# Optimization experiments

Hardware: AMD Instinct MI355X
Metric: run time of the kernel (lower is better)

The kernel has to match this reference:

```python
import jax, jax.numpy as jnp
import numpy as np
from jax import lax

MARGIN = 1.0
LAMDA = 0.003
EPS = 1e-9


def extract_features(f, idx):
    # f: (B,C,h,w); idx: (B,N,2) int with idx[...,0]=x, idx[...,1]=y -> (B*N, C)
    B, N = idx.shape[:2]
    b = jnp.arange(B)[:, None]
    x = idx[..., 0]
    y = idx[..., 1]
    g = f[b, :, y, x]  # (B, N, C)
    return g.reshape(B * N, f.shape[1])


def grad_axis(f, axis):
    # np.gradient along one axis: central differences, one-sided at edges
    fl = jnp.moveaxis(f, axis, 0)
    g = jnp.concatenate([
        fl[1:2] - fl[0:1],
        (fl[2:] - fl[:-2]) * 0.5,
        fl[-1:] - fl[-2:-1],
    ], axis=0)
    return jnp.moveaxis(g, 0, axis)


def contrastive(fa, fb, N, pos):
    diff = fa - fb
    if pos:
        return jnp.sum(diff * diff / N)
    m = jnp.maximum(MARGIN - diff, 0.0)
    return jnp.sum(m * m / N)


def gn_loss(f_t, fb, ub):
    # f_t: (B*N, C) target features; fb: (B,C,h,w); ub: (B,N,2) int matches
    B, N = ub.shape[:2]
    xs = ub  # deterministic stand-in for round(rand + ub) rejection sampling
    f_s = extract_features(fb, xs)
    r = f_s - f_t  # (BN, C)
    fbd = lax.stop_gradient(fb)  # original uses fb.detach() for gradients
    gy = grad_axis(fbd, 2)
    gx = grad_axis(fbd, 3)
    Jx = extract_features(gx, xs)  # (BN, C)
    Jy = extract_features(gy, xs)
    J = jnp.stack([Jx, Jy], axis=-1)  # (BN, C, 2)
    H = jnp.einsum('nci,ncj->nij', J, J) + EPS * jnp.eye(2, dtype=fb.dtype)
    b = jnp.einsum('nci,nc->ni', J, r)  # (BN, 2)
    xsf = xs.reshape(B * N, 2).astype(fb.dtype)
    miu = xsf - jnp.einsum('nij,nj->ni', jnp.linalg.inv(H), b)
    d = ub.reshape(B * N, 2).astype(fb.dtype) - miu
    e1 = 0.5 * jnp.sum(jnp.einsum('na,nab,nb->n', d, H, d))
    log_det = jnp.log(jnp.linalg.det(H))
    e2 = B * N * jnp.log(jnp.asarray(2.0 * np.pi, fb.dtype)) - 0.5 * jnp.sum(log_det)
    return e1 + e2


def gn_forward(F_a, F_b, ka, kb, na, nb):
    N = ka.shape[1]
    fa4 = extract_features(F_a[-1], ka)
    fb4 = extract_features(F_b[-1], kb)
    loss = 0.0
    for i in range(4):
        level = 2 ** (3 - i)
        if i == 3:
            fa_pos, fb_pos = fa4, fb4
        else:
            fa_pos = extract_features(F_a[i], ka // level)
            fb_pos = extract_features(F_b[i], kb // level)
        fa_neg = extract_features(F_a[i], na // level)
        fb_neg = extract_features(F_b[i], nb // level)
        loss_pos = contrastive(fa_pos, fb_pos, N, pos=True)
        loss_neg = contrastive(fa_neg, fb_neg, N, pos=False)
        loss_gn = gn_loss(fa_pos, F_b[i], kb // level)
        loss = loss_pos + loss_neg + LAMDA * loss_gn + loss
    return loss


def setup_inputs() -> dict:
    key = jax.random.key(0)
    ks = jax.random.split(key, 12)
    B, C, H, W, N = 4, 64, 256, 256, 512
    inp = {}
    for j, (name, s) in enumerate([
        ('fa0', 32), ('fa1', 64), ('fa2', 128), ('fa3', 256),
        ('fb0', 32), ('fb1', 64), ('fb2', 128), ('fb3', 256)]):
        inp[name] = jax.random.normal(ks[j], (B, C, s, s), dtype=jnp.float32)
    for j, name in enumerate(['ka', 'kb', 'na', 'nb']):
        inp[name] = jax.random.randint(ks[8 + j], (B, N, 2), 0, 256, dtype=jnp.int32)
    return inp


def reference(fa0, fa1, fa2, fa3, fb0, fb1, fb2, fb3, ka, kb, na, nb):
    F_a = [fa0, fa1, fa2, fa3]
    F_b = [fb0, fb1, fb2, fb3]
    return gn_forward(F_a, F_b, ka, kb, na, nb)
```

## Files before the change

kernel.cpp:

```cpp
#include <hip/hip_runtime.h>

#define MARGIN 1.0f
#define LAMDA  0.003f
#define EPS_H  1e-9f

#define E2_CONST (0.003f * 4.0f * 2048.0f * 1.8378770664093453f)

__device__ __forceinline__ float finalize_level(const float* v) {
    const float Hxx = v[2] + EPS_H;
    const float Hxy = v[3];
    const float Hyy = v[4] + EPS_H;
    const float bX  = v[5];
    const float bY  = v[6];
    const float det = Hxx * Hyy - Hxy * Hxy;
    const float e1  = 0.5f * (Hyy * bX * bX - 2.0f * Hxy * bX * bY + Hxx * bY * bY) / det;
    return (v[0] + v[1]) * (1.0f / 512.0f) + LAMDA * (e1 - 0.5f * logf(det));
}

__device__ __forceinline__ void gather7(
    const float* __restrict__ fa, const float* __restrict__ fb,
    int2 kA, int2 kB, int2 nA, int2 nB,
    int shift, int S, int plane, float* v)
{
    const int kax = kA.x >> shift, kay = kA.y >> shift;
    const int kbx = kB.x >> shift, kby = kB.y >> shift;
    const int nax = nA.x >> shift, nay = nA.y >> shift;
    const int nbx = nB.x >> shift, nby = nB.y >> shift;

    const int   xm = (kbx > 0)     ? kbx - 1 : 0;
    const int   xp = (kbx < S - 1) ? kbx + 1 : S - 1;
    const float sx = (kbx > 0 && kbx < S - 1) ? 0.5f : 1.0f;
    const int   ym = (kby > 0)     ? kby - 1 : 0;
    const int   yp = (kby < S - 1) ? kby + 1 : S - 1;
    const float sy = (kby > 0 && kby < S - 1) ? 0.5f : 1.0f;

    const float va  = fa[plane + kay * S + kax];
    const float vna = fa[plane + nay * S + nax];
    const float vb  = fb[plane + kby * S + kbx];
    const float vnb = fb[plane + nby * S + nbx];
    const float gxm = fb[plane + kby * S + xm];
    const float gxp = fb[plane + kby * S + xp];
    const float gym = fb[plane + ym * S + kbx];
    const float gyp = fb[plane + yp * S + kbx];

    const float Jx = (gxp - gxm) * sx;
    const float Jy = (gyp - gym) * sy;

    const float dpos = va - vb;
    const float dneg = vna - vnb;
    const float mneg = fmaxf(MARGIN - dneg, 0.0f);
    const float r    = vb - va;

    v[0] = dpos * dpos;
    v[1] = mneg * mneg;
    v[2] = Jx * Jx;
    v[3] = Jx * Jy;
    v[4] = Jy * Jy;
    v[5] = Jx * r;
    v[6] = Jy * r;
}

__global__ __launch_bounds__(64) void gn_task_kernel(
    const float* __restrict__ fa0, const float* __restrict__ fa1,
    const float* __restrict__ fa2, const float* __restrict__ fa3,
    const float* __restrict__ fb0, const float* __restrict__ fb1,
    const float* __restrict__ fb2, const float* __restrict__ fb3,
    const int* __restrict__ ka, const int* __restrict__ kb,
    const int* __restrict__ na, const int* __restrict__ nb,
    float* __restrict__ out)
{
    const int lane = threadIdx.x;
    const int n    = blockIdx.x;
    const int b    = n >> 9;

    const int2 kA = ((const int2*)ka)[n];
    const int2 kB = ((const int2*)kb)[n];
    const int2 nA = ((const int2*)na)[n];
    const int2 nB = ((const int2*)nb)[n];

    const int base = (b * 64 + lane);
    const int plane0 = base * (32 * 32);
    const int plane1 = base * (64 * 64);
    const int plane2 = base * (128 * 128);
    const int plane3 = base * (256 * 256);

    float v[28];
    gather7(fa0, fb0, kA, kB, nA, nB, 3, 32,  plane0, v);
    gather7(fa1, fb1, kA, kB, nA, nB, 2, 64,  plane1, v + 7);
    gather7(fa2, fb2, kA, kB, nA, nB, 1, 128, plane2, v + 14);
    gather7(fa3, fb3, kA, kB, nA, nB, 0, 256, plane3, v + 21);

    #pragma unroll
    for (int mask = 32; mask >= 1; mask >>= 1)
        #pragma unroll
        for (int t = 0; t < 28; ++t)
            v[t] += __shfl_xor(v[t], mask, 64);

    if (lane == 0) {
        float s = finalize_level(v) + finalize_level(v + 7)
                + finalize_level(v + 14) + finalize_level(v + 21);
        if (n == 0) s += E2_CONST;
        atomicAdd(out, s);
    }
}

extern "C" void kernel_launch(void* const* d_in, const int* in_sizes, int n_in,
                              void* d_out, int out_size, void* d_ws, size_t ws_size,
                              hipStream_t stream) {
    const float* fa0 = (const float*)d_in[0];
    const float* fa1 = (const float*)d_in[1];
    const float* fa2 = (const float*)d_in[2];
    const float* fa3 = (const float*)d_in[3];
    const float* fb0 = (const float*)d_in[4];
    const float* fb1 = (const float*)d_in[5];
    const float* fb2 = (const float*)d_in[6];
    const float* fb3 = (const float*)d_in[7];
    const int*   ka  = (const int*)d_in[8];
    const int*   kb  = (const int*)d_in[9];
    const int*   na  = (const int*)d_in[10];
    const int*   nb  = (const int*)d_in[11];

    float* out = (float*)d_out;
    hipMemsetAsync(out, 0, sizeof(float), stream);

    gn_task_kernel<<<2048, 64, 0, stream>>>(fa0, fa1, fa2, fa3,
                                            fb0, fb1, fb2, fb3,
                                            ka, kb, na, nb, out);
}
```

Before: 58.97 us.

## Split pyramid levels across waves and process two keypoints per block

```diff
diff --git a/kernel.cpp b/kernel.cpp
--- a/kernel.cpp
+++ b/kernel.cpp
@@ -60,7 +60,7 @@
     v[6] = Jy * r;
 }
 
-__global__ __launch_bounds__(64) void gn_task_kernel(
+__global__ __launch_bounds__(256) void gn_task_kernel(
     const float* __restrict__ fa0, const float* __restrict__ fa1,
     const float* __restrict__ fa2, const float* __restrict__ fa3,
     const float* __restrict__ fb0, const float* __restrict__ fb1,
@@ -69,37 +69,54 @@
     const int* __restrict__ na, const int* __restrict__ nb,
     float* __restrict__ out)
 {
-    const int lane = threadIdx.x;
-    const int n    = blockIdx.x;
-    const int b    = n >> 9;
+    __shared__ float wloss[4];
 
-    const int2 kA = ((const int2*)ka)[n];
-    const int2 kB = ((const int2*)kb)[n];
-    const int2 nA = ((const int2*)na)[n];
-    const int2 nB = ((const int2*)nb)[n];
+    const int wave  = threadIdx.x >> 6;
+    const int lane  = threadIdx.x & 63;
+    const int level = wave;
+    const int shift = 3 - level;
+    const int S     = 32 << level;
 
-    const int base = (b * 64 + lane);
-    const int plane0 = base * (32 * 32);
-    const int plane1 = base * (64 * 64);
-    const int plane2 = base * (128 * 128);
-    const int plane3 = base * (256 * 256);
+    const int n0 = blockIdx.x * 2;
+    const int n1 = n0 + 1;
+    const int b  = n0 >> 9;
 
-    float v[28];
-    gather7(fa0, fb0, kA, kB, nA, nB, 3, 32,  plane0, v);
-    gather7(fa1, fb1, kA, kB, nA, nB, 2, 64,  plane1, v + 7);
-    gather7(fa2, fb2, kA, kB, nA, nB, 1, 128, plane2, v + 14);
-    gather7(fa3, fb3, kA, kB, nA, nB, 0, 256, plane3, v + 21);
+    const float* fa; const float* fb;
+    switch (level) {
+        case 0:  fa = fa0; fb = fb0; break;
+        case 1:  fa = fa1; fb = fb1; break;
+        case 2:  fa = fa2; fb = fb2; break;
+        default: fa = fa3; fb = fb3; break;
+    }
+
+    const int2 kA0 = ((const int2*)ka)[n0];
+    const int2 kB0 = ((const int2*)kb)[n0];
+    const int2 nA0 = ((const int2*)na)[n0];
+    const int2 nB0 = ((const int2*)nb)[n0];
+    const int2 kA1 = ((const int2*)ka)[n1];
+    const int2 kB1 = ((const int2*)kb)[n1];
+    const int2 nA1 = ((const int2*)na)[n1];
+    const int2 nB1 = ((const int2*)nb)[n1];
+
+    const int plane = (b * 64 + lane) * (S * S);
+
+    float v[14];
+    gather7(fa, fb, kA0, kB0, nA0, nB0, shift, S, plane, v);
+    gather7(fa, fb, kA1, kB1, nA1, nB1, shift, S, plane, v + 7);
 
     #pragma unroll
     for (int mask = 32; mask >= 1; mask >>= 1)
         #pragma unroll
-        for (int t = 0; t < 28; ++t)
+        for (int t = 0; t < 14; ++t)
             v[t] += __shfl_xor(v[t], mask, 64);
 
-    if (lane == 0) {
-        float s = finalize_level(v) + finalize_level(v + 7)
-                + finalize_level(v + 14) + finalize_level(v + 21);
-        if (n == 0) s += E2_CONST;
+    if (lane == 0)
+        wloss[wave] = finalize_level(v) + finalize_level(v + 7);
+
+    __syncthreads();
+    if (threadIdx.x == 0) {
+        float s = wloss[0] + wloss[1] + wloss[2] + wloss[3];
+        if (blockIdx.x == 0) s += E2_CONST;
         atomicAdd(out, s);
     }
 }
@@ -123,7 +140,7 @@
     float* out = (float*)d_out;
     hipMemsetAsync(out, 0, sizeof(float), stream);
 
-    gn_task_kernel<<<2048, 64, 0, stream>>>(fa0, fa1, fa2, fa3,
-                                            fb0, fb1, fb2, fb3,
-                                            ka, kb, na, nb, out);
+    gn_task_kernel<<<1024, 256, 0, stream>>>(fa0, fa1, fa2, fa3,
+                                             fb0, fb1, fb2, fb3,
+                                             ka, kb, na, nb, out);
 }
```

After: 52.61 us. 10.8% less time.
